# Kernel tuning notes

Measured on AMD Instinct MI355X. Metric: run time of the kernel, lower is better.

Reference implementation:

```python
import jax, jax.numpy as jnp
import numpy as np

# TT-linear: in_features=1024 -> out_features=4096
IN_DIMS = (8, 8, 4, 4)      # m1..m4, prod = 1024
OUT_DIMS = (8, 8, 8, 8)     # n1..n4, prod = 4096
RANKS = (1, 16, 16, 16, 1)  # r0..r4
IN_FEATURES = 1024
OUT_FEATURES = 4096
BATCH, SEQ = 4, 1024


def _init_core(key, shape):
    # uniform(-1,1)/sqrt(fan_in-ish), matching the original's uniform-style init scale
    fan = shape[0] * shape[1]
    return (2.0 * jax.random.uniform(key, shape, dtype=jnp.float32) - 1.0) / np.sqrt(fan).astype(np.float32)


def setup_inputs() -> dict:
    key = jax.random.key(0)
    ks = jax.random.split(key, 6)
    x = jax.random.normal(ks[0], (BATCH, SEQ, IN_FEATURES), dtype=jnp.float32)
    core0 = _init_core(ks[1], (1, 8, 8, 16))    # [r0, m1, n1, r1]
    core1 = _init_core(ks[2], (16, 8, 8, 16))   # [r1, m2, n2, r2]
    core2 = _init_core(ks[3], (16, 4, 8, 16))   # [r2, m3, n3, r3]
    core3 = _init_core(ks[4], (16, 4, 8, 1))    # [r3, m4, n4, r4]
    bias = (2.0 * jax.random.uniform(ks[5], (OUT_FEATURES,), dtype=jnp.float32) - 1.0) / np.sqrt(OUT_FEATURES).astype(np.float32)
    return {"x": x, "core0": core0, "core1": core1, "core2": core2, "core3": core3, "bias": bias}


def reference(x, core0, core1, core2, core3, bias):
    lead = x.shape[:-1]
    # split the feature axis into TT input factors: [T, m1, m2, m3, m4]
    t = x.reshape((-1,) + IN_DIMS)
    c0 = core0[0]        # [m1, n1, r1]   (boundary rank r0 = 1 squeezed)
    c3 = core3[..., 0]   # [r3, m4, n4]   (boundary rank r4 = 1 squeezed)
    # sequential TT core chain: absorb one m_k, emit one n_k per step
    t = jnp.einsum('tijkl,ixp->tjklxp', t, c0)      # [T, m2,m3,m4, n1, r1]
    t = jnp.einsum('tjklxp,pjyq->tklxyq', t, core1)  # [T, m3,m4, n1,n2, r2]
    t = jnp.einsum('tklxyq,qkzr->tlxyzr', t, core2)  # [T, m4, n1,n2,n3, r3]
    t = jnp.einsum('tlxyzr,rlw->txyzw', t, c3)       # [T, n1,n2,n3,n4]
    y = t.reshape(lead + (OUT_FEATURES,)) + bias
    return y
```

## Files before the change

kernel.cpp:

```cpp
#include <hip/hip_runtime.h>
#include <hip/hip_bf16.h>
#include <cstdint>


typedef __bf16 bf16x8 __attribute__((ext_vector_type(8)));
typedef float f32x4 __attribute__((ext_vector_type(4)));

__device__ __forceinline__ void g2lds16(const void* g, void* l) {
    __builtin_amdgcn_global_load_lds(
        (const __attribute__((address_space(1))) void*)g,
        (__attribute__((address_space(3))) void*)l,
        16, 0, 0);
}

__global__ __launch_bounds__(256) void prep(
    const float* __restrict__ x, __bf16* __restrict__ xb,
    const float* __restrict__ c0, const float* __restrict__ c1,
    const float* __restrict__ c2, const float* __restrict__ c3,
    __bf16* __restrict__ wt) {
    const int b = blockIdx.x;
    const int t = threadIdx.x;
    if (b < 2048) {
        const int i = (b * 256 + t) * 8;
        float4 a0 = *(const float4*)(x + i);
        float4 a1 = *(const float4*)(x + i + 4);
        bf16x8 o;
        o[0] = (__bf16)a0.x; o[1] = (__bf16)a0.y; o[2] = (__bf16)a0.z; o[3] = (__bf16)a0.w;
        o[4] = (__bf16)a1.x; o[5] = (__bf16)a1.y; o[6] = (__bf16)a1.z; o[7] = (__bf16)a1.w;
        *(bf16x8*)(xb + i) = o;
        return;
    }
    __shared__ float t12[4][16];
    __shared__ float t123[4][512];
    __shared__ float c3s[512];
    #pragma unroll
    for (int i = t; i < 512; i += 256) c3s[i] = c3[i];
    const int s = t >> 6;
    const int lane = t & 63;
    const int g = (b - 2048) * 4 + s;
    const int m1 = g >> 9, n1 = (g >> 6) & 7, m2 = (g >> 3) & 7, n2 = g & 7;
    __syncthreads();
    if (lane < 16) {
        const int r2 = lane;
        float sum = 0.f;
        #pragma unroll
        for (int r1 = 0; r1 < 16; ++r1)
            sum += c0[(m1 * 8 + n1) * 16 + r1] * c1[((r1 * 8 + m2) * 8 + n2) * 16 + r2];
        t12[s][r2] = sum;
    }
    __syncthreads();
    #pragma unroll
    for (int idx = lane; idx < 512; idx += 64) {
        const int m3 = idx >> 7, n3 = (idx >> 4) & 7, r3 = idx & 15;
        float sum = 0.f;
        #pragma unroll
        for (int r2 = 0; r2 < 16; ++r2)
            sum += t12[s][r2] * c2[((r2 * 4 + m3) * 8 + n3) * 16 + r3];
        t123[s][(m3 * 8 + n3) * 16 + r3] = sum;
    }
    __syncthreads();
    const int n3 = lane >> 3, n4 = lane & 7;
    const int n = ((n1 * 8 + n2) * 8 + n3) * 8 + n4;
    const int kbase = (m1 * 8 + m2) * 16;
    float v[16];
    #pragma unroll
    for (int e = 0; e < 16; ++e) v[e] = 0.f;
    #pragma unroll
    for (int m3 = 0; m3 < 4; ++m3) {
        #pragma unroll
        for (int r3 = 0; r3 < 16; ++r3) {
            const float tv = t123[s][(m3 * 8 + n3) * 16 + r3];
            #pragma unroll
            for (int m4 = 0; m4 < 4; ++m4)
                v[m3 * 4 + m4] += tv * c3s[(r3 * 4 + m4) * 8 + n4];
        }
    }
    bf16x8 lo, hi;
    #pragma unroll
    for (int e = 0; e < 8; ++e) { lo[e] = (__bf16)v[e]; hi[e] = (__bf16)v[8 + e]; }
    *(bf16x8*)(wt + (size_t)n * 1024 + kbase)     = lo;
    *(bf16x8*)(wt + (size_t)n * 1024 + kbase + 8) = hi;
}

__global__ __launch_bounds__(256) void tt_gemm(
    const __bf16* __restrict__ A, const __bf16* __restrict__ B,
    const float* __restrict__ bias, float* __restrict__ C) {
    constexpr int K = 1024, N = 4096;
    __shared__ __bf16 sA[128 * 64];
    __shared__ __bf16 sB[128 * 64];
    const int t = threadIdx.x;
    const int lane = t & 63;
    const int wave = t >> 6;
    const int wm = (wave >> 1) * 64;
    const int wn = (wave & 1) * 64;
    const int xcd = blockIdx.x & 7;
    const int lid = blockIdx.x >> 3;
    const int bm = (lid & 31) * 128;
    const int bn = (xcd * 4 + (lid >> 5)) * 128;
    const int l15 = lane & 15, lh = lane >> 4;
    const int swz = l15 & 7;

    f32x4 acc[4][4] = {};

    for (int k0 = 0; k0 < K; k0 += 64) {
        __syncthreads();
        #pragma unroll
        for (int i = 0; i < 4; ++i) {
            const int c = t + i * 256;
            const int r = c >> 3;
            const int gc = (c & 7) ^ (r & 7);
            g2lds16(A + (size_t)(bm + r) * K + k0 + gc * 8, (char*)sA + (size_t)c * 16);
            g2lds16(B + (size_t)(bn + r) * K + k0 + gc * 8, (char*)sB + (size_t)c * 16);
        }
        asm volatile("s_waitcnt vmcnt(0)" ::: "memory");
        __syncthreads();
        #pragma unroll
        for (int kk = 0; kk < 2; ++kk) {
            const int coff = ((kk * 4 + lh) ^ swz) * 16;
            bf16x8 af[4], bfr[4];
            #pragma unroll
            for (int mi = 0; mi < 4; ++mi)
                af[mi] = *(const bf16x8*)((const char*)sA + (size_t)(wm + mi * 16 + l15) * 128 + coff);
            #pragma unroll
            for (int ni = 0; ni < 4; ++ni)
                bfr[ni] = *(const bf16x8*)((const char*)sB + (size_t)(wn + ni * 16 + l15) * 128 + coff);
            #pragma unroll
            for (int mi = 0; mi < 4; ++mi)
                #pragma unroll
                for (int ni = 0; ni < 4; ++ni)
                    acc[mi][ni] = __builtin_amdgcn_mfma_f32_16x16x32_bf16(
                        af[mi], bfr[ni], acc[mi][ni], 0, 0, 0);
        }
    }

    #pragma unroll
    for (int ni = 0; ni < 4; ++ni) {
        const int col = bn + wn + ni * 16 + l15;
        const float bv = bias[col];
        #pragma unroll
        for (int mi = 0; mi < 4; ++mi) {
            const int row0 = bm + wm + mi * 16 + lh * 4;
            const f32x4 v = acc[mi][ni];
            #pragma unroll
            for (int r = 0; r < 4; ++r)
                C[(size_t)(row0 + r) * N + col] = v[r] + bv;
        }
    }
}

extern "C" void kernel_launch(void* const* d_in, const int* in_sizes, int n_in,
                              void* d_out, int out_size, void* d_ws, size_t ws_size,
                              hipStream_t stream) {
    const float* x    = (const float*)d_in[0];
    const float* c0   = (const float*)d_in[1];
    const float* c1   = (const float*)d_in[2];
    const float* c2   = (const float*)d_in[3];
    const float* c3   = (const float*)d_in[4];
    const float* bias = (const float*)d_in[5];
    float* out = (float*)d_out;

    __bf16* xb = (__bf16*)d_ws;
    __bf16* wt = xb + (size_t)4096 * 1024;

    prep<<<3072, 256, 0, stream>>>(x, xb, c0, c1, c2, c3, wt);
    tt_gemm<<<1024, 256, 0, stream>>>(xb, wt, bias, out);
}
```

Measured before the change: 142.1 us.

## Fuse weight reconstruction and GEMM into one persistent kernel with grid barrier

Merges the two kernels into a single launch. Each block first builds its slice of the dense TT weight, then waits at a global atomic-counter barrier, then runs the GEMM. The separate bf16 copy of x is gone: each block converts fp32 x to bf16 on the fly while loading the A tile into LDS, which removes one full read/write pass over the activations and a kernel launch. The A tile now goes through registers instead of async global-to-LDS loads, and the x conversion is repeated by every column-tile block. The grid barrier assumes all 1024 blocks are co-resident and has a spin timeout that could silently break correctness otherwise. A memset for the counter is added, and block-to-tile mapping changes (drops XCD-aware swizzle).

```diff
diff --git a/kernel.cpp b/kernel.cpp
--- a/kernel.cpp
+++ b/kernel.cpp
@@ -13,104 +13,110 @@
         16, 0, 0);
 }
 
-__global__ __launch_bounds__(256) void prep(
-    const float* __restrict__ x, __bf16* __restrict__ xb,
+__global__ __launch_bounds__(256, 4) void tt_fused(
+    const float* __restrict__ x,
     const float* __restrict__ c0, const float* __restrict__ c1,
     const float* __restrict__ c2, const float* __restrict__ c3,
-    __bf16* __restrict__ wt) {
-    const int b = blockIdx.x;
+    const float* __restrict__ bias,
+    __bf16* __restrict__ wt, unsigned* __restrict__ ctr,
+    float* __restrict__ C) {
+    __shared__ __align__(16) char smem[32768];
     const int t = threadIdx.x;
-    if (b < 2048) {
-        const int i = (b * 256 + t) * 8;
-        float4 a0 = *(const float4*)(x + i);
-        float4 a1 = *(const float4*)(x + i + 4);
-        bf16x8 o;
-        o[0] = (__bf16)a0.x; o[1] = (__bf16)a0.y; o[2] = (__bf16)a0.z; o[3] = (__bf16)a0.w;
-        o[4] = (__bf16)a1.x; o[5] = (__bf16)a1.y; o[6] = (__bf16)a1.z; o[7] = (__bf16)a1.w;
-        *(bf16x8*)(xb + i) = o;
-        return;
+    const int blk = blockIdx.x;
+
+    {
+        float* t12  = (float*)smem;
+        float* t123 = (float*)(smem + 256);
+        float* c3s  = (float*)(smem + 256 + 8192);
+        for (int i = t; i < 512; i += 256) c3s[i] = c3[i];
+        const int s = t >> 6, lane = t & 63;
+        const int g = blk * 4 + s;
+        const int m1 = g >> 9, n1 = (g >> 6) & 7, m2 = (g >> 3) & 7, n2 = g & 7;
+        __syncthreads();
+        if (lane < 16) {
+            float sum = 0.f;
+            #pragma unroll
+            for (int r1 = 0; r1 < 16; ++r1)
+                sum += c0[(m1 * 8 + n1) * 16 + r1] * c1[((r1 * 8 + m2) * 8 + n2) * 16 + lane];
+            t12[s * 16 + lane] = sum;
+        }
+        __syncthreads();
+        #pragma unroll
+        for (int idx = lane; idx < 512; idx += 64) {
+            const int m3 = idx >> 7, n3 = (idx >> 4) & 7, r3 = idx & 15;
+            float sum = 0.f;
+            #pragma unroll
+            for (int r2 = 0; r2 < 16; ++r2)
+                sum += t12[s * 16 + r2] * c2[((r2 * 4 + m3) * 8 + n3) * 16 + r3];
+            t123[s * 512 + (m3 * 8 + n3) * 16 + r3] = sum;
+        }
+        __syncthreads();
+        const int n3 = lane >> 3, n4 = lane & 7;
+        const int n = ((n1 * 8 + n2) * 8 + n3) * 8 + n4;
+        const int kbase = (m1 * 8 + m2) * 16;
+        float v[16];
+        #pragma unroll
+        for (int e = 0; e < 16; ++e) v[e] = 0.f;
+        #pragma unroll
+        for (int m3 = 0; m3 < 4; ++m3)
+            #pragma unroll
+            for (int r3 = 0; r3 < 16; ++r3) {
+                const float tv = t123[s * 512 + (m3 * 8 + n3) * 16 + r3];
+                #pragma unroll
+                for (int m4 = 0; m4 < 4; ++m4)
+                    v[m3 * 4 + m4] += tv * c3s[(r3 * 4 + m4) * 8 + n4];
+            }
+        bf16x8 lo, hi;
+        #pragma unroll
+        for (int e = 0; e < 8; ++e) { lo[e] = (__bf16)v[e]; hi[e] = (__bf16)v[8 + e]; }
+        *(bf16x8*)(wt + (size_t)n * 1024 + kbase)     = lo;
+        *(bf16x8*)(wt + (size_t)n * 1024 + kbase + 8) = hi;
     }
-    __shared__ float t12[4][16];
-    __shared__ float t123[4][512];
-    __shared__ float c3s[512];
-    #pragma unroll
-    for (int i = t; i < 512; i += 256) c3s[i] = c3[i];
-    const int s = t >> 6;
-    const int lane = t & 63;
-    const int g = (b - 2048) * 4 + s;
-    const int m1 = g >> 9, n1 = (g >> 6) & 7, m2 = (g >> 3) & 7, n2 = g & 7;
+
+    __threadfence();
     __syncthreads();
-    if (lane < 16) {
-        const int r2 = lane;
-        float sum = 0.f;
-        #pragma unroll
-        for (int r1 = 0; r1 < 16; ++r1)
-            sum += c0[(m1 * 8 + n1) * 16 + r1] * c1[((r1 * 8 + m2) * 8 + n2) * 16 + r2];
-        t12[s][r2] = sum;
+    if (t == 0) {
+        __hip_atomic_fetch_add(ctr, 1u, __ATOMIC_ACQ_REL, __HIP_MEMORY_SCOPE_AGENT);
+        int spins = 0;
+        while (__hip_atomic_load(ctr, __ATOMIC_ACQUIRE, __HIP_MEMORY_SCOPE_AGENT) < 1024u) {
+            __builtin_amdgcn_s_sleep(4);
+            if (++spins > (1 << 20)) break;
+        }
     }
     __syncthreads();
-    #pragma unroll
-    for (int idx = lane; idx < 512; idx += 64) {
-        const int m3 = idx >> 7, n3 = (idx >> 4) & 7, r3 = idx & 15;
-        float sum = 0.f;
-        #pragma unroll
-        for (int r2 = 0; r2 < 16; ++r2)
-            sum += t12[s][r2] * c2[((r2 * 4 + m3) * 8 + n3) * 16 + r3];
-        t123[s][(m3 * 8 + n3) * 16 + r3] = sum;
-    }
-    __syncthreads();
-    const int n3 = lane >> 3, n4 = lane & 7;
-    const int n = ((n1 * 8 + n2) * 8 + n3) * 8 + n4;
-    const int kbase = (m1 * 8 + m2) * 16;
-    float v[16];
-    #pragma unroll
-    for (int e = 0; e < 16; ++e) v[e] = 0.f;
-    #pragma unroll
-    for (int m3 = 0; m3 < 4; ++m3) {
-        #pragma unroll
-        for (int r3 = 0; r3 < 16; ++r3) {
-            const float tv = t123[s][(m3 * 8 + n3) * 16 + r3];
-            #pragma unroll
-            for (int m4 = 0; m4 < 4; ++m4)
-                v[m3 * 4 + m4] += tv * c3s[(r3 * 4 + m4) * 8 + n4];
-        }
-    }
-    bf16x8 lo, hi;
-    #pragma unroll
-    for (int e = 0; e < 8; ++e) { lo[e] = (__bf16)v[e]; hi[e] = (__bf16)v[8 + e]; }
-    *(bf16x8*)(wt + (size_t)n * 1024 + kbase)     = lo;
-    *(bf16x8*)(wt + (size_t)n * 1024 + kbase + 8) = hi;
-}
 
-__global__ __launch_bounds__(256) void tt_gemm(
-    const __bf16* __restrict__ A, const __bf16* __restrict__ B,
-    const float* __restrict__ bias, float* __restrict__ C) {
-    constexpr int K = 1024, N = 4096;
-    __shared__ __bf16 sA[128 * 64];
-    __shared__ __bf16 sB[128 * 64];
-    const int t = threadIdx.x;
-    const int lane = t & 63;
-    const int wave = t >> 6;
-    const int wm = (wave >> 1) * 64;
-    const int wn = (wave & 1) * 64;
-    const int xcd = blockIdx.x & 7;
-    const int lid = blockIdx.x >> 3;
-    const int bm = (lid & 31) * 128;
-    const int bn = (xcd * 4 + (lid >> 5)) * 128;
+    __bf16* sAp = (__bf16*)smem;
+    __bf16* sBp = (__bf16*)(smem + 16384);
+    const int lane = t & 63, wave = t >> 6;
+    const int wm = (wave >> 1) * 64, wn = (wave & 1) * 64;
+    const int bm = (blk >> 5) * 128;
+    const int bn = (blk & 31) * 128;
     const int l15 = lane & 15, lh = lane >> 4;
     const int swz = l15 & 7;
 
     f32x4 acc[4][4] = {};
 
-    for (int k0 = 0; k0 < K; k0 += 64) {
+    for (int k0 = 0; k0 < 1024; k0 += 64) {
         __syncthreads();
         #pragma unroll
         for (int i = 0; i < 4; ++i) {
             const int c = t + i * 256;
             const int r = c >> 3;
             const int gc = (c & 7) ^ (r & 7);
-            g2lds16(A + (size_t)(bm + r) * K + k0 + gc * 8, (char*)sA + (size_t)c * 16);
-            g2lds16(B + (size_t)(bn + r) * K + k0 + gc * 8, (char*)sB + (size_t)c * 16);
+            g2lds16(wt + (size_t)(bn + r) * 1024 + k0 + gc * 8, (char*)sBp + (size_t)c * 16);
+        }
+        #pragma unroll
+        for (int i = 0; i < 4; ++i) {
+            const int c = t + i * 256;
+            const int r = c >> 3;
+            const int lc = c & 7;
+            const float4* p = (const float4*)(x + (size_t)(bm + r) * 1024 + k0 + lc * 8);
+            float4 a0 = p[0], a1 = p[1];
+            bf16x8 o;
+            o[0] = (__bf16)a0.x; o[1] = (__bf16)a0.y; o[2] = (__bf16)a0.z; o[3] = (__bf16)a0.w;
+            o[4] = (__bf16)a1.x; o[5] = (__bf16)a1.y; o[6] = (__bf16)a1.z; o[7] = (__bf16)a1.w;
+            const int pc = lc ^ (r & 7);
+            *(bf16x8*)((char*)sAp + (size_t)(r * 8 + pc) * 16) = o;
         }
         asm volatile("s_waitcnt vmcnt(0)" ::: "memory");
         __syncthreads();
@@ -120,10 +126,10 @@
             bf16x8 af[4], bfr[4];
             #pragma unroll
             for (int mi = 0; mi < 4; ++mi)
-                af[mi] = *(const bf16x8*)((const char*)sA + (size_t)(wm + mi * 16 + l15) * 128 + coff);
+                af[mi] = *(const bf16x8*)((const char*)sAp + (size_t)(wm + mi * 16 + l15) * 128 + coff);
             #pragma unroll
             for (int ni = 0; ni < 4; ++ni)
-                bfr[ni] = *(const bf16x8*)((const char*)sB + (size_t)(wn + ni * 16 + l15) * 128 + coff);
+                bfr[ni] = *(const bf16x8*)((const char*)sBp + (size_t)(wn + ni * 16 + l15) * 128 + coff);
             #pragma unroll
             for (int mi = 0; mi < 4; ++mi)
                 #pragma unroll
@@ -140,10 +146,10 @@
         #pragma unroll
         for (int mi = 0; mi < 4; ++mi) {
             const int row0 = bm + wm + mi * 16 + lh * 4;
-            const f32x4 v = acc[mi][ni];
+            const f32x4 vv = acc[mi][ni];
             #pragma unroll
             for (int r = 0; r < 4; ++r)
-                C[(size_t)(row0 + r) * N + col] = v[r] + bv;
+                C[(size_t)(row0 + r) * 4096 + col] = vv[r] + bv;
         }
     }
 }
@@ -159,9 +165,9 @@
     const float* bias = (const float*)d_in[5];
     float* out = (float*)d_out;
 
-    __bf16* xb = (__bf16*)d_ws;
-    __bf16* wt = xb + (size_t)4096 * 1024;
+    __bf16* wt = (__bf16*)d_ws;
+    unsigned* ctr = (unsigned*)((char*)d_ws + (size_t)4096 * 1024 * 2);
 
-    prep<<<3072, 256, 0, stream>>>(x, xb, c0, c1, c2, c3, wt);
-    tt_gemm<<<1024, 256, 0, stream>>>(xb, wt, bias, out);
+    hipMemsetAsync(ctr, 0, 4, stream);
+    tt_fused<<<1024, 256, 0, stream>>>(x, c0, c1, c2, c3, bias, wt, ctr, out);
 }
```

New measurement: 353.5 us. 149% more time.

## Double-buffer GEMM LDS tiles with K=32 stages and prefetch overlap

Applied to the files above, without the earlier changes.

Restructures the GEMM main loop to use two LDS buffers of K=32 slices, issuing the next slice's global-to-LDS loads before computing on the current one, so memory latency overlaps with MFMA work. The XOR swizzle is adapted to the 64-byte rows, and the XCD-aware block-to-tile mapping is replaced with a plain row-major mapping. The loop now synchronises every 32 K elements instead of every 64, which doubles barrier count, and dropping the XCD remap may reduce L2 locality.

```diff
diff --git a/kernel.cpp b/kernel.cpp
--- a/kernel.cpp
+++ b/kernel.cpp
@@ -86,51 +86,60 @@
     const __bf16* __restrict__ A, const __bf16* __restrict__ B,
     const float* __restrict__ bias, float* __restrict__ C) {
     constexpr int K = 1024, N = 4096;
-    __shared__ __bf16 sA[128 * 64];
-    __shared__ __bf16 sB[128 * 64];
+    __shared__ __bf16 sA[2][128 * 32];
+    __shared__ __bf16 sB[2][128 * 32];
     const int t = threadIdx.x;
     const int lane = t & 63;
     const int wave = t >> 6;
     const int wm = (wave >> 1) * 64;
     const int wn = (wave & 1) * 64;
-    const int xcd = blockIdx.x & 7;
-    const int lid = blockIdx.x >> 3;
-    const int bm = (lid & 31) * 128;
-    const int bn = (xcd * 4 + (lid >> 5)) * 128;
+    const int bm = (blockIdx.x >> 5) * 128;
+    const int bn = (blockIdx.x & 31) * 128;
     const int l15 = lane & 15, lh = lane >> 4;
-    const int swz = l15 & 7;
+    const int coff = ((lh ^ ((l15 >> 1) & 3))) * 16;
+
+    const int c1 = t, c2 = t + 256;
+    const int r1c = c1 >> 2, gc1 = (c1 & 3) ^ ((r1c >> 1) & 3);
+    const int r2c = c2 >> 2, gc2 = (c2 & 3) ^ ((r2c >> 1) & 3);
+    const __bf16* gA1 = A + (size_t)(bm + r1c) * K + gc1 * 8;
+    const __bf16* gA2 = A + (size_t)(bm + r2c) * K + gc2 * 8;
+    const __bf16* gB1 = B + (size_t)(bn + r1c) * K + gc1 * 8;
+    const __bf16* gB2 = B + (size_t)(bn + r2c) * K + gc2 * 8;
 
     f32x4 acc[4][4] = {};
 
-    for (int k0 = 0; k0 < K; k0 += 64) {
-        __syncthreads();
+    g2lds16(gA1, (char*)sA[0] + (size_t)c1 * 16);
+    g2lds16(gA2, (char*)sA[0] + (size_t)c2 * 16);
+    g2lds16(gB1, (char*)sB[0] + (size_t)c1 * 16);
+    g2lds16(gB2, (char*)sB[0] + (size_t)c2 * 16);
+
+    for (int i = 0; i < 32; ++i) {
+        const int p = i & 1;
+        asm volatile("s_barrier" ::: "memory");
+        if (i < 31) {
+            const int k1 = (i + 1) * 32;
+            g2lds16(gA1 + k1, (char*)sA[p ^ 1] + (size_t)c1 * 16);
+            g2lds16(gA2 + k1, (char*)sA[p ^ 1] + (size_t)c2 * 16);
+            g2lds16(gB1 + k1, (char*)sB[p ^ 1] + (size_t)c1 * 16);
+            g2lds16(gB2 + k1, (char*)sB[p ^ 1] + (size_t)c2 * 16);
+            asm volatile("s_waitcnt vmcnt(4)" ::: "memory");
+        } else {
+            asm volatile("s_waitcnt vmcnt(0)" ::: "memory");
+        }
+        asm volatile("s_barrier" ::: "memory");
+        bf16x8 af[4], bfr[4];
         #pragma unroll
-        for (int i = 0; i < 4; ++i) {
-            const int c = t + i * 256;
-            const int r = c >> 3;
-            const int gc = (c & 7) ^ (r & 7);
-            g2lds16(A + (size_t)(bm + r) * K + k0 + gc * 8, (char*)sA + (size_t)c * 16);
-            g2lds16(B + (size_t)(bn + r) * K + k0 + gc * 8, (char*)sB + (size_t)c * 16);
-        }
-        asm volatile("s_waitcnt vmcnt(0)" ::: "memory");
-        __syncthreads();
+        for (int mi = 0; mi < 4; ++mi)
+            af[mi] = *(const bf16x8*)((const char*)sA[p] + (size_t)(wm + mi * 16 + l15) * 64 + coff);
         #pragma unroll
-        for (int kk = 0; kk < 2; ++kk) {
-            const int coff = ((kk * 4 + lh) ^ swz) * 16;
-            bf16x8 af[4], bfr[4];
-            #pragma unroll
-            for (int mi = 0; mi < 4; ++mi)
-                af[mi] = *(const bf16x8*)((const char*)sA + (size_t)(wm + mi * 16 + l15) * 128 + coff);
+        for (int ni = 0; ni < 4; ++ni)
+            bfr[ni] = *(const bf16x8*)((const char*)sB[p] + (size_t)(wn + ni * 16 + l15) * 64 + coff);
+        #pragma unroll
+        for (int mi = 0; mi < 4; ++mi)
             #pragma unroll
             for (int ni = 0; ni < 4; ++ni)
-                bfr[ni] = *(const bf16x8*)((const char*)sB + (size_t)(wn + ni * 16 + l15) * 128 + coff);
-            #pragma unroll
-            for (int mi = 0; mi < 4; ++mi)
-                #pragma unroll
-                for (int ni = 0; ni < 4; ++ni)
-                    acc[mi][ni] = __builtin_amdgcn_mfma_f32_16x16x32_bf16(
-                        af[mi], bfr[ni], acc[mi][ni], 0, 0, 0);
-        }
+                acc[mi][ni] = __builtin_amdgcn_mfma_f32_16x16x32_bf16(
+                    af[mi], bfr[ni], acc[mi][ni], 0, 0, 0);
     }
 
     #pragma unroll
```

After: 148.9 us. 1.05x slower.
